# Optimization experiments

Measured on AMD Instinct MI355X. Metric: run time of the kernel, lower is better.

The kernel has to match this reference:

```python
import jax, jax.numpy as jnp
import numpy as np

LENGTH = 50          # side length of square patch (init kwarg)
HALF = LENGTH // 2   # fill_rectangle uses patch half-sizes around center
FILL_VALUE = 0.0     # fill_mode='constant'


def setup_inputs() -> dict:
    key = jax.random.key(0)
    k_img, k_lab, k_ch, k_cw = jax.random.split(key, 4)
    B, H, W, C = 64, 512, 512, 3
    images = jax.random.normal(k_img, (B, H, W, C), dtype=jnp.float32)
    labels = jax.random.randint(k_lab, (B,), 0, 1000, dtype=jnp.int32)
    center_h = jax.random.randint(k_ch, (B,), 0, H, dtype=jnp.int32)
    center_w = jax.random.randint(k_cw, (B,), 0, W, dtype=jnp.int32)
    return {"images": images, "labels": labels, "center_h": center_h, "center_w": center_w}


def reference(images, labels, center_h, center_w):
    # Vectorized equivalent of tf.map_fn(fill_rectangle, ...):
    # per-sample rectangle [cy-HALF, cy+HALF) x [cx-HALF, cx+HALF),
    # clipped implicitly to image bounds by the index comparisons.
    B, H, W, C = images.shape
    rows = jnp.arange(H)[None, :, None]                # [1, H, 1]
    cols = jnp.arange(W)[None, None, :]                # [1, 1, W]
    ch = center_h[:, None, None]                       # [B, 1, 1]
    cw = center_w[:, None, None]
    mask = ((rows >= ch - HALF) & (rows < ch + HALF) &
            (cols >= cw - HALF) & (cols < cw + HALF))  # [B, H, W]
    out = jnp.where(mask[..., None], jnp.float32(FILL_VALUE), images)
    return out, labels
```

## Files before the change

### kernel.cpp

```cpp
#include <hip/hip_runtime.h>


#define HALF   25
#define BATCH  64
#define IMG_H  512
#define IMG_W  512
#define IMG_C  3
#define IMG_ELEMS ((size_t)BATCH * IMG_H * IMG_W * IMG_C)

__global__ void cutout_zero_and_labels(float* __restrict__ out,
                                       const int* __restrict__ center_h,
                                       const int* __restrict__ center_w,
                                       const int* __restrict__ labels,
                                       float* __restrict__ out_labels) {
    const int b = blockIdx.y;

    if (blockIdx.x == 0 && blockIdx.y == 0 && threadIdx.x < BATCH) {
        out_labels[threadIdx.x] = (float)labels[threadIdx.x];
    }

    const int r = center_h[b] - HALF + (int)blockIdx.x;
    if (r < 0 || r >= IMG_H) return;

    const int cw = center_w[b];
    const int c0 = max(0, cw - HALF);
    const int c1 = min(IMG_W, cw + HALF);
    const int n  = (c1 - c0) * IMG_C;
    if (n <= 0) return;

    const size_t base = (((size_t)b * IMG_H + r) * IMG_W + c0) * IMG_C;
    for (int i = threadIdx.x; i < n; i += blockDim.x) {
        out[base + i] = 0.0f;
    }
}

extern "C" void kernel_launch(void* const* d_in, const int* in_sizes, int n_in,
                              void* d_out, int out_size, void* d_ws, size_t ws_size,
                              hipStream_t stream) {
    const float* images   = (const float*)d_in[0];
    const int*   labels   = (const int*)  d_in[1];
    const int*   center_h = (const int*)  d_in[2];
    const int*   center_w = (const int*)  d_in[3];
    float* out = (float*)d_out;

    hipMemcpyAsync(out, images, IMG_ELEMS * sizeof(float),
                   hipMemcpyDeviceToDevice, stream);

    dim3 grid(2 * HALF, BATCH);
    cutout_zero_and_labels<<<grid, 192, 0, stream>>>(
        out, center_h, center_w, labels, out + IMG_ELEMS);
}
```

Baseline: 330.1 us.

## Fuse image copy and cutout masking into one vectorized streaming kernel

Replaces the device-to-device memcpy followed by a patch-zeroing kernel with a single kernel. It reads each float4 of the image, computes per-element mask membership from pixel indices, and writes the masked value. This removes one launch and the serialized second pass over the patch region. In exchange it adds per-element index math and center lookups to a bandwidth-bound copy.

```diff
diff --git a/kernel.cpp b/kernel.cpp
--- a/kernel.cpp
+++ b/kernel.cpp
@@ -6,32 +6,56 @@
 #define IMG_H  512
 #define IMG_W  512
 #define IMG_C  3
-#define IMG_ELEMS ((size_t)BATCH * IMG_H * IMG_W * IMG_C)
+#define N_PIX  (BATCH * IMG_H * IMG_W)
+#define N_ELEM ((size_t)N_PIX * IMG_C)
+#define N_VEC  (N_ELEM / 4)
 
-__global__ void cutout_zero_and_labels(float* __restrict__ out,
-                                       const int* __restrict__ center_h,
-                                       const int* __restrict__ center_w,
-                                       const int* __restrict__ labels,
-                                       float* __restrict__ out_labels) {
-    const int b = blockIdx.y;
+__device__ __forceinline__ bool inbox(unsigned p,
+                                      const int* __restrict__ ch,
+                                      const int* __restrict__ cw) {
+    const int w = (int)(p & (IMG_W - 1));
+    const int h = (int)((p >> 9) & (IMG_H - 1));
+    const int b = (int)(p >> 18);
+    const int chb = ch[b];
+    const int cwb = cw[b];
+    return (h >= chb - HALF) & (h < chb + HALF) &
+           (w >= cwb - HALF) & (w < cwb + HALF);
+}
 
-    if (blockIdx.x == 0 && blockIdx.y == 0 && threadIdx.x < BATCH) {
+__global__ __launch_bounds__(256) void cutout_fused(
+    const float4* __restrict__ in,
+    float4* __restrict__ out,
+    const int* __restrict__ center_h,
+    const int* __restrict__ center_w,
+    const int* __restrict__ labels,
+    float* __restrict__ out_labels)
+{
+    const unsigned vid = blockIdx.x * 256u + threadIdx.x;
+
+    if (blockIdx.x == 0 && threadIdx.x < BATCH) {
         out_labels[threadIdx.x] = (float)labels[threadIdx.x];
     }
 
-    const int r = center_h[b] - HALF + (int)blockIdx.x;
-    if (r < 0 || r >= IMG_H) return;
+    float4 v = in[vid];
 
-    const int cw = center_w[b];
-    const int c0 = max(0, cw - HALF);
-    const int c1 = min(IMG_W, cw + HALF);
-    const int n  = (c1 - c0) * IMG_C;
-    if (n <= 0) return;
+    const unsigned idx4 = vid * 4u;
+    const unsigned pi   = idx4 / 3u;
+    const unsigned rem  = idx4 - pi * 3u;
 
-    const size_t base = (((size_t)b * IMG_H + r) * IMG_W + c0) * IMG_C;
-    for (int i = threadIdx.x; i < n; i += blockDim.x) {
-        out[base + i] = 0.0f;
-    }
+    const bool m0 = inbox(pi,     center_h, center_w);
+    const bool m1 = inbox(pi + 1, center_h, center_w);
+
+    const bool me0 = m0;
+    const bool me1 = (rem >= 2) ? m1 : m0;
+    const bool me2 = (rem >= 1) ? m1 : m0;
+    const bool me3 = m1;
+
+    if (me0) v.x = 0.0f;
+    if (me1) v.y = 0.0f;
+    if (me2) v.z = 0.0f;
+    if (me3) v.w = 0.0f;
+
+    out[vid] = v;
 }
 
 extern "C" void kernel_launch(void* const* d_in, const int* in_sizes, int n_in,
@@ -43,10 +67,8 @@
     const int*   center_w = (const int*)  d_in[3];
     float* out = (float*)d_out;
 
-    hipMemcpyAsync(out, images, IMG_ELEMS * sizeof(float),
-                   hipMemcpyDeviceToDevice, stream);
-
-    dim3 grid(2 * HALF, BATCH);
-    cutout_zero_and_labels<<<grid, 192, 0, stream>>>(
-        out, center_h, center_w, labels, out + IMG_ELEMS);
+    const unsigned nblocks = N_VEC / 256;
+    cutout_fused<<<nblocks, 256, 0, stream>>>(
+        (const float4*)images, (float4*)out,
+        center_h, center_w, labels, out + N_ELEM);
 }
```

Result: faster. 321.4 us (-2.6%).
